# Kernel tuning notes

Hardware: AMD Instinct MI355X
Metric: run time of the kernel (lower is better)

The kernel has to match this reference:

```python
import jax, jax.numpy as jnp
import numpy as np

B, H, W_DIM, C = 16, 128, 128, 256

def setup_inputs() -> dict:
    key = jax.random.key(0)
    k1, k2, k3 = jax.random.split(key, 3)
    grid = jax.random.normal(k1, (B, H, W_DIM, C), dtype=jnp.float32)
    # nn.Linear(2C, C): weight [C, 2C], bias [C]; store transposed for x @ W
    W = jax.random.normal(k2, (2 * C, C), dtype=jnp.float32) * (1.0 / np.sqrt(2 * C))
    b = jax.random.normal(k3, (C,), dtype=jnp.float32) * 0.01
    return {"grid": grid, "W": W, "b": b}

def reference(grid, W, b):
    # cumulative max along width (axis=2) and height (axis=1)
    x_cummax = jax.lax.cummax(grid, axis=2)
    y_cummax = jax.lax.cummax(grid, axis=1)
    result = jnp.concatenate([x_cummax, y_cummax], axis=-1)  # [B,H,W,2C]
    return result @ W + b  # [B,H,W,C]
```

## Files before the change

kernel.cpp:

```cpp
#include <hip/hip_runtime.h>
#include <hip/hip_fp16.h>

#define BB 16
#define HH 128
#define WW 128
#define CC 256

typedef __attribute__((ext_vector_type(8))) short s16x8;
typedef __attribute__((ext_vector_type(8))) unsigned short u16x8;
typedef __attribute__((ext_vector_type(4))) float f32x4;
typedef __attribute__((ext_vector_type(4))) int i32x4;

__device__ static inline unsigned short f2bf(float x) {
    union { float f; unsigned u; } v; v.f = x;
    unsigned r = v.u + 0x7fffu + ((v.u >> 16) & 1u);
    return (unsigned short)(r >> 16);
}
__device__ static inline float bf2f(unsigned short u) {
    union { unsigned u; float f; } v; v.u = (unsigned)u << 16; return v.f;
}
__device__ static inline unsigned short h2u(__half h) {
    unsigned short u; __builtin_memcpy(&u, &h, 2); return u;
}
__device__ static inline float u2f16(unsigned short u) {
    __half h; __builtin_memcpy(&h, &u, 2); return __half2float(h);
}
__device__ static inline int sidx(int row, int col) {
    return row * 256 + (((col >> 3) ^ (row & 7)) << 3) + (col & 7);
}

__global__ __launch_bounds__(256) void conv_w_kernel(const float* __restrict__ Wf,
                                                     unsigned short* __restrict__ Wt) {
    const int i = blockIdx.x * 256 + threadIdx.x;
    const int n = i & 255, k = i >> 8;
    const int hy = k >> 8, g = (k >> 3) & 31, j = k & 7;
    Wt[hy * 65536 + ((size_t)(g * 256 + n) << 3) + j] = f2bf(Wf[i]);
}

__device__ __forceinline__ void scan_half(const float* __restrict__ src, size_t st,
                                          unsigned short* __restrict__ As, int c, int row0) {
    float buf[8], nxt[8];
    const float* p = src;
    #pragma unroll
    for (int j = 0; j < 8; ++j) buf[j] = p[(size_t)j * st];
    __builtin_amdgcn_sched_group_barrier(0x20, 8, 0);
    p += 8 * st;
    float run = -3.4e38f;
    const int chi = c >> 3, clo = c & 7;
    #pragma unroll
    for (int g = 0; g < 8; ++g) {
        if (g < 7) {
            #pragma unroll
            for (int j = 0; j < 8; ++j) nxt[j] = p[(size_t)j * st];
            __builtin_amdgcn_sched_group_barrier(0x20, 8, 0);
            p += 8 * st;
        }
        #pragma unroll
        for (int j = 0; j < 8; ++j) {
            run = fmaxf(run, buf[j]);
            const int row = row0 + g * 8 + j;
            As[row * 256 + ((chi ^ (row & 7)) << 3) + clo] = f2bf(run);
        }
        if (g < 7) {
            #pragma unroll
            for (int j = 0; j < 8; ++j) buf[j] = nxt[j];
        }
    }
}

__device__ __forceinline__ void carry_fix(unsigned short* __restrict__ As, int c) {
    const unsigned short cb = As[sidx(63, c)];
    const float cf = bf2f(cb);
    #pragma unroll 8
    for (int j = 0; j < 64; ++j) {
        const int ix = sidx(64 + j, c);
        const unsigned short v = As[ix];
        As[ix] = (bf2f(v) >= cf) ? v : cb;
    }
}

__device__ __forceinline__ void gemm_stage(unsigned short* __restrict__ As,
                                           const s16x8* __restrict__ Wv, int t) {
    const int lane = t & 63, wid = t >> 6;
    const int wr = wid >> 2, wn = wid & 3;
    f32x4 acc[4][4];
    #pragma unroll
    for (int i = 0; i < 4; ++i)
        #pragma unroll
        for (int j = 0; j < 4; ++j) acc[i][j] = (f32x4){0.f, 0.f, 0.f, 0.f};

    #pragma unroll
    for (int q = 0; q < 8; ++q) {
        const int g = q * 4 + (lane >> 4);
        s16x8 af[4], bf[4];
        #pragma unroll
        for (int fm = 0; fm < 4; ++fm) {
            const int row = wr * 64 + fm * 16 + (lane & 15);
            af[fm] = *(const s16x8*)(As + row * 256 + ((g ^ (row & 7)) << 3));
        }
        #pragma unroll
        for (int fn = 0; fn < 4; ++fn)
            bf[fn] = Wv[g * 256 + wn * 64 + fn * 16 + (lane & 15)];
        #pragma unroll
        for (int fm = 0; fm < 4; ++fm)
            #pragma unroll
            for (int fn = 0; fn < 4; ++fn)
                acc[fm][fn] = __builtin_amdgcn_mfma_f32_16x16x32_bf16(
                    af[fm], bf[fn], acc[fm][fn], 0, 0, 0);
    }
    __syncthreads();
    #pragma unroll
    for (int fn = 0; fn < 4; ++fn) {
        const int col = wn * 64 + fn * 16 + (lane & 15);
        #pragma unroll
        for (int fm = 0; fm < 4; ++fm) {
            const int rbase = wr * 64 + fm * 16 + ((lane >> 4) << 2);
            #pragma unroll
            for (int r = 0; r < 4; ++r)
                As[sidx(rbase + r, col)] = h2u(__float2half(acc[fm][fn][r]));
        }
    }
    __syncthreads();
}

__global__ __launch_bounds__(512, 3) void hscan_gemm_kernel(const float* __restrict__ grid,
                                                            const unsigned short* __restrict__ Wt,
                                                            unsigned short* __restrict__ partial) {
    __shared__ unsigned short As[32768];
    const int t = threadIdx.x;
    const int c = t & 255, s = t >> 8;
    const int b = blockIdx.x >> 7;
    const int w = blockIdx.x & 127;

    const float* base = grid + ((size_t)(b * 128 + s * 64) * 128 + w) * 256 + c;
    scan_half(base, 32768, As, c, s * 64);
    __syncthreads();
    if (s == 1) carry_fix(As, c);
    __syncthreads();

    gemm_stage(As, (const s16x8*)(Wt + 65536), t);

    #pragma unroll
    for (int it = 0; it < 8; ++it) {
        const int f = it * 4096 + t * 8;
        const int row = f >> 8, col = f & 255;
        const i32x4 v = *(const i32x4*)(As + sidx(row, col));
        *(i32x4*)(partial + (((size_t)b * 128 + row) * 128 + w) * 256 + col) = v;
    }
}

__global__ __launch_bounds__(512, 3) void wscan_gemm_kernel(const float* __restrict__ grid,
                                                            const unsigned short* __restrict__ Wt,
                                                            const unsigned short* __restrict__ partial,
                                                            const float* __restrict__ bias,
                                                            float* __restrict__ out) {
    __shared__ unsigned short As[32768];
    const int t = threadIdx.x;
    const int c = t & 255, s = t >> 8;
    const size_t bh = blockIdx.x;

    const float* base = grid + (bh * 128 + (size_t)(s * 64)) * 256 + c;
    scan_half(base, 256, As, c, s * 64);
    __syncthreads();
    if (s == 1) carry_fix(As, c);
    __syncthreads();

    gemm_stage(As, (const s16x8*)Wt, t);

    const int colf = (t * 8) & 255;
    float bv[8];
    #pragma unroll
    for (int k = 0; k < 8; ++k) bv[k] = bias[colf + k];

    #pragma unroll
    for (int it = 0; it < 8; ++it) {
        const int f = it * 4096 + t * 8;
        const int row = f >> 8, col = f & 255;
        const u16x8 lv = *(const u16x8*)(As + sidx(row, col));
        const size_t gi = (bh * 128 + row) * 256 + col;
        const u16x8 pv = *(const u16x8*)(partial + gi);
        f32x4 o0, o1;
        #pragma unroll
        for (int k = 0; k < 4; ++k)
            o0[k] = u2f16((unsigned short)lv[k]) + u2f16((unsigned short)pv[k]) + bv[k];
        #pragma unroll
        for (int k = 0; k < 4; ++k)
            o1[k] = u2f16((unsigned short)lv[4 + k]) + u2f16((unsigned short)pv[4 + k]) + bv[4 + k];
        *(f32x4*)(out + gi)     = o0;
        *(f32x4*)(out + gi + 4) = o1;
    }
}

extern "C" void kernel_launch(void* const* d_in, const int* in_sizes, int n_in,
                              void* d_out, int out_size, void* d_ws, size_t ws_size,
                              hipStream_t stream) {
    const float* grid = (const float*)d_in[0];
    const float* Wf   = (const float*)d_in[1];
    const float* bias = (const float*)d_in[2];
    float* out        = (float*)d_out;

    unsigned short* partial = (unsigned short*)d_ws;
    unsigned short* Wt      = (unsigned short*)((char*)d_ws + (size_t)134217728);

    conv_w_kernel<<<512, 256, 0, stream>>>(Wf, Wt);
    hscan_gemm_kernel<<<2048, 512, 0, stream>>>(grid, Wt, partial);
    wscan_gemm_kernel<<<2048, 512, 0, stream>>>(grid, Wt, partial, bias, out);
}
```

Measured before the change: 268.9 us.

## Split scans into eight 16-row segments with float4 loads and carry propagation

```diff
diff --git a/kernel.cpp b/kernel.cpp
--- a/kernel.cpp
+++ b/kernel.cpp
@@ -27,6 +27,9 @@
 }
 __device__ static inline int sidx(int row, int col) {
     return row * 256 + (((col >> 3) ^ (row & 7)) << 3) + (col & 7);
+}
+__device__ static inline int sidx4(int row, int c4) {
+    return row * 256 + (((c4 >> 1) ^ (row & 7)) << 3) + (c4 & 1) * 4;
 }
 
 __global__ __launch_bounds__(256) void conv_w_kernel(const float* __restrict__ Wf,
@@ -37,45 +40,59 @@
     Wt[hy * 65536 + ((size_t)(g * 256 + n) << 3) + j] = f2bf(Wf[i]);
 }
 
-__device__ __forceinline__ void scan_half(const float* __restrict__ src, size_t st,
-                                          unsigned short* __restrict__ As, int c, int row0) {
-    float buf[8], nxt[8];
-    const float* p = src;
-    #pragma unroll
-    for (int j = 0; j < 8; ++j) buf[j] = p[(size_t)j * st];
+__device__ __forceinline__ void scan16_to_lds(const float4* __restrict__ base, size_t st,
+                                              unsigned short* __restrict__ As,
+                                              unsigned short* __restrict__ smax,
+                                              int c4, int s) {
+    const int row0 = s * 16;
+    float4 buf[8], nxt[8];
+    #pragma unroll
+    for (int j = 0; j < 8; ++j) buf[j] = base[(size_t)j * st];
     __builtin_amdgcn_sched_group_barrier(0x20, 8, 0);
-    p += 8 * st;
-    float run = -3.4e38f;
-    const int chi = c >> 3, clo = c & 7;
-    #pragma unroll
-    for (int g = 0; g < 8; ++g) {
-        if (g < 7) {
-            #pragma unroll
-            for (int j = 0; j < 8; ++j) nxt[j] = p[(size_t)j * st];
-            __builtin_amdgcn_sched_group_barrier(0x20, 8, 0);
-            p += 8 * st;
-        }
-        #pragma unroll
-        for (int j = 0; j < 8; ++j) {
-            run = fmaxf(run, buf[j]);
-            const int row = row0 + g * 8 + j;
-            As[row * 256 + ((chi ^ (row & 7)) << 3) + clo] = f2bf(run);
-        }
-        if (g < 7) {
-            #pragma unroll
-            for (int j = 0; j < 8; ++j) buf[j] = nxt[j];
-        }
-    }
-}
-
-__device__ __forceinline__ void carry_fix(unsigned short* __restrict__ As, int c) {
-    const unsigned short cb = As[sidx(63, c)];
-    const float cf = bf2f(cb);
-    #pragma unroll 8
-    for (int j = 0; j < 64; ++j) {
-        const int ix = sidx(64 + j, c);
-        const unsigned short v = As[ix];
-        As[ix] = (bf2f(v) >= cf) ? v : cb;
+    #pragma unroll
+    for (int j = 0; j < 8; ++j) nxt[j] = base[(size_t)(8 + j) * st];
+    __builtin_amdgcn_sched_group_barrier(0x20, 8, 0);
+    float4 run = make_float4(-3.4e38f, -3.4e38f, -3.4e38f, -3.4e38f);
+    #pragma unroll
+    for (int j = 0; j < 8; ++j) {
+        run.x = fmaxf(run.x, buf[j].x); run.y = fmaxf(run.y, buf[j].y);
+        run.z = fmaxf(run.z, buf[j].z); run.w = fmaxf(run.w, buf[j].w);
+        ushort4 o; o.x = f2bf(run.x); o.y = f2bf(run.y); o.z = f2bf(run.z); o.w = f2bf(run.w);
+        *(ushort4*)(As + sidx4(row0 + j, c4)) = o;
+    }
+    #pragma unroll
+    for (int j = 0; j < 8; ++j) {
+        run.x = fmaxf(run.x, nxt[j].x); run.y = fmaxf(run.y, nxt[j].y);
+        run.z = fmaxf(run.z, nxt[j].z); run.w = fmaxf(run.w, nxt[j].w);
+        ushort4 o; o.x = f2bf(run.x); o.y = f2bf(run.y); o.z = f2bf(run.z); o.w = f2bf(run.w);
+        *(ushort4*)(As + sidx4(row0 + 8 + j, c4)) = o;
+    }
+    ushort4 sm; sm.x = f2bf(run.x); sm.y = f2bf(run.y); sm.z = f2bf(run.z); sm.w = f2bf(run.w);
+    *(ushort4*)(smax + s * 256 + c4 * 4) = sm;
+}
+
+__device__ __forceinline__ void carry_apply(unsigned short* __restrict__ As,
+                                            const unsigned short* __restrict__ smax,
+                                            int c4, int s) {
+    if (s == 0) return;
+    float4 cf = make_float4(-3.4e38f, -3.4e38f, -3.4e38f, -3.4e38f);
+    for (int k = 0; k < s; ++k) {
+        const ushort4 m = *(const ushort4*)(smax + k * 256 + c4 * 4);
+        cf.x = fmaxf(cf.x, bf2f(m.x)); cf.y = fmaxf(cf.y, bf2f(m.y));
+        cf.z = fmaxf(cf.z, bf2f(m.z)); cf.w = fmaxf(cf.w, bf2f(m.w));
+    }
+    ushort4 cb; cb.x = f2bf(cf.x); cb.y = f2bf(cf.y); cb.z = f2bf(cf.z); cb.w = f2bf(cf.w);
+    const int row0 = s * 16;
+    #pragma unroll
+    for (int r = 0; r < 16; ++r) {
+        unsigned short* pp = As + sidx4(row0 + r, c4);
+        ushort4 v = *(ushort4*)(pp);
+        ushort4 o;
+        o.x = (bf2f(v.x) >= cf.x) ? v.x : cb.x;
+        o.y = (bf2f(v.y) >= cf.y) ? v.y : cb.y;
+        o.z = (bf2f(v.z) >= cf.z) ? v.z : cb.z;
+        o.w = (bf2f(v.w) >= cf.w) ? v.w : cb.w;
+        *(ushort4*)(pp) = o;
     }
 }
 
@@ -123,19 +140,20 @@
     __syncthreads();
 }
 
-__global__ __launch_bounds__(512, 3) void hscan_gemm_kernel(const float* __restrict__ grid,
+__global__ __launch_bounds__(512, 4) void hscan_gemm_kernel(const float* __restrict__ grid,
                                                             const unsigned short* __restrict__ Wt,
                                                             unsigned short* __restrict__ partial) {
     __shared__ unsigned short As[32768];
+    __shared__ unsigned short smax[2048];
     const int t = threadIdx.x;
-    const int c = t & 255, s = t >> 8;
+    const int c4 = t & 63, s = t >> 6;
     const int b = blockIdx.x >> 7;
     const int w = blockIdx.x & 127;
 
-    const float* base = grid + ((size_t)(b * 128 + s * 64) * 128 + w) * 256 + c;
-    scan_half(base, 32768, As, c, s * 64);
-    __syncthreads();
-    if (s == 1) carry_fix(As, c);
+    const float4* base = (const float4*)(grid + ((size_t)(b * 128 + s * 16) * 128 + w) * 256) + c4;
+    scan16_to_lds(base, 8192, As, smax, c4, s);
+    __syncthreads();
+    carry_apply(As, smax, c4, s);
     __syncthreads();
 
     gemm_stage(As, (const s16x8*)(Wt + 65536), t);
@@ -149,20 +167,21 @@
     }
 }
 
-__global__ __launch_bounds__(512, 3) void wscan_gemm_kernel(const float* __restrict__ grid,
+__global__ __launch_bounds__(512, 4) void wscan_gemm_kernel(const float* __restrict__ grid,
                                                             const unsigned short* __restrict__ Wt,
                                                             const unsigned short* __restrict__ partial,
                                                             const float* __restrict__ bias,
                                                             float* __restrict__ out) {
     __shared__ unsigned short As[32768];
+    __shared__ unsigned short smax[2048];
     const int t = threadIdx.x;
-    const int c = t & 255, s = t >> 8;
+    const int c4 = t & 63, s = t >> 6;
     const size_t bh = blockIdx.x;
 
-    const float* base = grid + (bh * 128 + (size_t)(s * 64)) * 256 + c;
-    scan_half(base, 256, As, c, s * 64);
-    __syncthreads();
-    if (s == 1) carry_fix(As, c);
+    const float4* base = (const float4*)(grid + (bh * 128 + (size_t)(s * 16)) * 256) + c4;
+    scan16_to_lds(base, 64, As, smax, c4, s);
+    __syncthreads();
+    carry_apply(As, smax, c4, s);
     __syncthreads();
 
     gemm_stage(As, (const s16x8*)Wt, t);
```

Result: faster. 257.8 us (-4.1%).
